# Kernel optimization log

Measured on AMD Instinct MI355X. Metric: run time of the kernel, lower is better.

Reference implementation:

```python
import jax, jax.numpy as jnp
import numpy as np

TEMPERATURE = 0.5
EPS = 1e-8  # torch CosineSimilarity eps


def setup_inputs() -> dict:
    key = jax.random.key(0)
    k1, k2 = jax.random.split(key)
    N, D = 4096, 256
    z1 = jax.random.normal(k1, (N, D), dtype=jnp.float32)
    z2 = jax.random.normal(k2, (N, D), dtype=jnp.float32)
    return {"z1": z1, "z2": z2}


def reference(z1, z2):
    N = z1.shape[0]
    z = jnp.concatenate([z1, z2], axis=0)  # [2N, D]
    # cosine similarity = normalized dot products (GEMM instead of O(N^2 D) broadcast)
    norm = jnp.linalg.norm(z, axis=-1, keepdims=True)
    zn = z / jnp.maximum(norm, EPS)
    sim = (zn @ zn.T) / TEMPERATURE  # [2N, 2N]
    # mask self-similarity on the diagonal
    idx = jnp.arange(2 * N)
    sim = jnp.where(idx[:, None] == idx[None, :], -jnp.inf, sim)
    # target[i] = (i - N) mod 2N  (arange(2N).roll(N))
    target = jnp.roll(idx, N)
    logp = jax.nn.log_softmax(sim, axis=-1)
    loss = -jnp.mean(logp[idx, target])
    return loss
```

## Files before the change

### kernel.cpp

```cpp
#include <hip/hip_runtime.h>

typedef __bf16 bf16x8 __attribute__((ext_vector_type(8)));
typedef float f32x4 __attribute__((ext_vector_type(4)));

#define TWO_LOG2E 2.88539008177792681f

#define GLOADLDS16(g, l) __builtin_amdgcn_global_load_lds(                     \
    (const __attribute__((address_space(1))) void*)(g),                        \
    (__attribute__((address_space(3))) void*)(l), 16, 0, 0)

__device__ __forceinline__ unsigned f2bf(float f) {
    unsigned u = __float_as_uint(f);
    return (u + 0x7FFFu + ((u >> 16) & 1u)) >> 16;
}

__global__ void __launch_bounds__(256) normalize_kernel(
    const float* __restrict__ z1, const float* __restrict__ z2,
    unsigned short* __restrict__ zn, float* __restrict__ S, float* __restrict__ out)
{
    if (blockIdx.x < 32) S[(blockIdx.x << 8) + threadIdx.x] = 0.f;
    if (blockIdx.x == 32 && threadIdx.x == 0) out[0] = 0.f;

    const int wave = threadIdx.x >> 6, lane = threadIdx.x & 63;
    const int row = (blockIdx.x << 2) + wave;
    const float* src = (row < 4096) ? (z1 + row * 256) : (z2 + (row - 4096) * 256);
    float4 v = ((const float4*)src)[lane];
    float ss = v.x * v.x + v.y * v.y + v.z * v.z + v.w * v.w;
#pragma unroll
    for (int m = 32; m > 0; m >>= 1) ss += __shfl_xor(ss, m, 64);
    float sc = 1.0f / fmaxf(sqrtf(ss), 1e-8f);
    uint2 w;
    w.x = f2bf(v.x * sc) | (f2bf(v.y * sc) << 16);
    w.y = f2bf(v.z * sc) | (f2bf(v.w * sc) << 16);
    *(uint2*)(zn + row * 256 + (lane << 2)) = w;
}

__global__ void __launch_bounds__(512, 4) simexp_kernel(
    const unsigned short* __restrict__ zn, float* __restrict__ S)
{
    __shared__ __align__(16) unsigned short Bs[4][2048];

    const int tid = threadIdx.x;
    const int wv = tid >> 6, lane = tid & 63;
    const int q = lane >> 4, n16 = lane & 15;
    const int g = wv >> 2, wl = wv & 3;
    const int bid = blockIdx.x;
    const int run   = ((bid & 7) << 1) | ((bid >> 3) & 1);
    const int strip = bid >> 4;
    const int rowBase = strip << 8;
    const int colRun  = run << 9;
    const int rowW = rowBase + (wv << 5);

    bf16x8 a[2][8];
#pragma unroll
    for (int rt = 0; rt < 2; ++rt)
#pragma unroll
        for (int ks = 0; ks < 8; ++ks)
            a[rt][ks] = *(const bf16x8*)(zn + ((rowW + (rt << 4) + n16) << 8)
                                            + (ks << 5) + (q << 3));

    auto stage = [&](int m) {
        const int colBase = colRun + ((m >> 2) << 5);
        const int koff = (m & 3) << 6;
        unsigned short* base = &Bs[m & 3][0];
        int s = (wl << 6) + lane;
        int c = s >> 3, d = s & 7;
        int k8 = d ^ (c & 7);
        GLOADLDS16(zn + ((colBase + c) << 8) + koff + (k8 << 3), base + (s << 3));
    };

    float rs[2][4];
#pragma unroll
    for (int i = 0; i < 2; ++i)
#pragma unroll
        for (int j = 0; j < 4; ++j) rs[i][j] = 0.f;

    f32x4 acc[2][2];
    auto consume = [&](int kc) {
        const unsigned short* bb = &Bs[kc & 3][0];
#pragma unroll
        for (int ks = 0; ks < 2; ++ks) {
            bf16x8 bf[2];
#pragma unroll
            for (int ct = 0; ct < 2; ++ct) {
                int c  = (ct << 4) + n16;
                int k8 = ((ks << 2) + q) ^ (c & 7);
                bf[ct] = *(const bf16x8*)(bb + (((c << 3) + k8) << 3));
            }
#pragma unroll
            for (int rt = 0; rt < 2; ++rt)
#pragma unroll
                for (int ct = 0; ct < 2; ++ct)
                    acc[rt][ct] = __builtin_amdgcn_mfma_f32_16x16x32_bf16(
                        a[rt][(kc << 1) + ks], bf[ct], acc[rt][ct], 0, 0, 0);
        }
    };
    auto zacc = [&]() {
#pragma unroll
        for (int rt = 0; rt < 2; ++rt)
#pragma unroll
            for (int ct = 0; ct < 2; ++ct) acc[rt][ct] = (f32x4){0.f, 0.f, 0.f, 0.f};
    };
    auto epilogue = [&]() {
#pragma unroll
        for (int rt = 0; rt < 2; ++rt)
#pragma unroll
            for (int ct = 0; ct < 2; ++ct)
#pragma unroll
                for (int r = 0; r < 4; ++r)
                    rs[rt][r] += __builtin_amdgcn_exp2f(acc[rt][ct][r] * TWO_LOG2E);
    };

    if (g == 0) stage(0); else stage(1);

    for (int cc = 0; cc < 15; ++cc) {
        zacc();
#pragma unroll
        for (int kc = 0; kc < 4; ++kc) {
            if ((kc & 1) == g) {
                stage((cc << 2) + kc + 2);
                asm volatile("s_waitcnt vmcnt(1)" ::: "memory");
            }
            __builtin_amdgcn_s_barrier();
            asm volatile("" ::: "memory");
            consume(kc);
        }
        epilogue();
    }
    zacc();
    if (g == 0) { stage(62); asm volatile("s_waitcnt vmcnt(1)" ::: "memory"); }
    __builtin_amdgcn_s_barrier();
    asm volatile("" ::: "memory");
    consume(0);
    if (g == 1) { stage(63); asm volatile("s_waitcnt vmcnt(1)" ::: "memory"); }
    __builtin_amdgcn_s_barrier();
    asm volatile("" ::: "memory");
    consume(1);
    if (g == 0) { asm volatile("s_waitcnt vmcnt(0)" ::: "memory"); }
    __builtin_amdgcn_s_barrier();
    asm volatile("" ::: "memory");
    consume(2);
    if (g == 1) { asm volatile("s_waitcnt vmcnt(0)" ::: "memory"); }
    __builtin_amdgcn_s_barrier();
    asm volatile("" ::: "memory");
    consume(3);
    epilogue();

#pragma unroll
    for (int rt = 0; rt < 2; ++rt)
#pragma unroll
        for (int r = 0; r < 4; ++r) {
            float s = rs[rt][r];
            s += __shfl_xor(s, 1, 64);
            s += __shfl_xor(s, 2, 64);
            s += __shfl_xor(s, 4, 64);
            s += __shfl_xor(s, 8, 64);
            if (n16 == 0) atomicAdd(&S[rowW + (rt << 4) + (q << 2) + r], s);
        }
}

__global__ void __launch_bounds__(256) finish_kernel(
    const unsigned short* __restrict__ zn, const float* __restrict__ S,
    float* __restrict__ out)
{
    __shared__ float vals[16];
    const int tid = threadIdx.x, lane = tid & 63, wave = tid >> 6;
    const int q = lane >> 4, n16 = lane & 15;
    const int rib = (wave << 2) + q;
    const int row = (blockIdx.x << 4) + rib;
    const int tar = (row + 4096) & 8191;

    float drr = 0.f, drt = 0.f;
#pragma unroll
    for (int i = 0; i < 4; ++i) {
        int k = (i << 6) + (n16 << 2);
        uint2 ur = *(const uint2*)(zn + (row << 8) + k);
        uint2 ut = *(const uint2*)(zn + (tar << 8) + k);
        float a0 = __uint_as_float(ur.x << 16),  a1 = __uint_as_float(ur.x & 0xFFFF0000u);
        float a2 = __uint_as_float(ur.y << 16),  a3 = __uint_as_float(ur.y & 0xFFFF0000u);
        float b0 = __uint_as_float(ut.x << 16),  b1 = __uint_as_float(ut.x & 0xFFFF0000u);
        float b2 = __uint_as_float(ut.y << 16),  b3 = __uint_as_float(ut.y & 0xFFFF0000u);
        drr += a0 * a0 + a1 * a1 + a2 * a2 + a3 * a3;
        drt += a0 * b0 + a1 * b1 + a2 * b2 + a3 * b3;
    }
#pragma unroll
    for (int m = 1; m <= 8; m <<= 1) {
        drr += __shfl_xor(drr, m, 64);
        drt += __shfl_xor(drt, m, 64);
    }
    if (n16 == 0) {
        float Sv = S[row] - __builtin_amdgcn_exp2f(drr * TWO_LOG2E);
        vals[rib] = 0.693147180559945f * __builtin_amdgcn_logf(Sv) - 2.0f * drt;
    }
    __syncthreads();
    if (tid == 0) {
        float s = 0.f;
#pragma unroll
        for (int i = 0; i < 16; ++i) s += vals[i];
        atomicAdd(out, s * (1.0f / 8192.0f));
    }
}

extern "C" void kernel_launch(void* const* d_in, const int* in_sizes, int n_in,
                              void* d_out, int out_size, void* d_ws, size_t ws_size,
                              hipStream_t stream)
{
    const float* z1 = (const float*)d_in[0];
    const float* z2 = (const float*)d_in[1];
    unsigned short* zn = (unsigned short*)d_ws;
    float* S = (float*)((char*)d_ws + 8192 * 256 * sizeof(unsigned short));
    float* out = (float*)d_out;

    normalize_kernel<<<2048, 256, 0, stream>>>(z1, z2, zn, S, out);
    simexp_kernel<<<512, 512, 0, stream>>>(zn, S);
    finish_kernel<<<512, 256, 0, stream>>>(zn, S, out);
}
```

Before: 101.6 us.

## Software-pipeline LDS fragment reads against MFMAs and raise MFMA priority

Splits the consume step into a fragment read from LDS and an MFMA step, double-buffering the B fragments so the LDS reads for chunk kc overlap the MFMAs for chunk kc-1. The epilogue exp and the accumulator reset move to the start of the next column chunk. MFMA blocks are wrapped in s_setprio to favour matrix issue. In exchange it uses more registers for the extra fragment buffer and adds explicit lgkmcnt waits before each barrier, which could reduce occupancy or serialise work.

New measurement: 135.7 us. +33.5%, slower.

```diff
diff --git a/kernel.cpp b/kernel.cpp
--- a/kernel.cpp
+++ b/kernel.cpp
@@ -76,24 +76,36 @@
         for (int j = 0; j < 4; ++j) rs[i][j] = 0.f;
 
     f32x4 acc[2][2];
-    auto consume = [&](int kc) {
+    bf16x8 bfP[2][2], bfN[2][2];
+
+    auto readfrags = [&](int kc) {
         const unsigned short* bb = &Bs[kc & 3][0];
 #pragma unroll
-        for (int ks = 0; ks < 2; ++ks) {
-            bf16x8 bf[2];
+        for (int ks = 0; ks < 2; ++ks)
 #pragma unroll
             for (int ct = 0; ct < 2; ++ct) {
                 int c  = (ct << 4) + n16;
                 int k8 = ((ks << 2) + q) ^ (c & 7);
-                bf[ct] = *(const bf16x8*)(bb + (((c << 3) + k8) << 3));
+                bfN[ks][ct] = *(const bf16x8*)(bb + (((c << 3) + k8) << 3));
             }
+    };
+    auto mfmastep = [&](int kcP) {
+        __builtin_amdgcn_s_setprio(1);
+#pragma unroll
+        for (int ks = 0; ks < 2; ++ks)
 #pragma unroll
             for (int rt = 0; rt < 2; ++rt)
 #pragma unroll
                 for (int ct = 0; ct < 2; ++ct)
                     acc[rt][ct] = __builtin_amdgcn_mfma_f32_16x16x32_bf16(
-                        a[rt][(kc << 1) + ks], bf[ct], acc[rt][ct], 0, 0, 0);
-        }
+                        a[rt][(kcP << 1) + ks], bfP[ks][ct], acc[rt][ct], 0, 0, 0);
+        __builtin_amdgcn_s_setprio(0);
+    };
+    auto rotate = [&]() {
+#pragma unroll
+        for (int ks = 0; ks < 2; ++ks)
+#pragma unroll
+            for (int ct = 0; ct < 2; ++ct) bfP[ks][ct] = bfN[ks][ct];
     };
     auto zacc = [&]() {
 #pragma unroll
@@ -111,39 +123,58 @@
                     rs[rt][r] += __builtin_amdgcn_exp2f(acc[rt][ct][r] * TWO_LOG2E);
     };
 
+    zacc();
     if (g == 0) stage(0); else stage(1);
 
     for (int cc = 0; cc < 15; ++cc) {
-        zacc();
 #pragma unroll
         for (int kc = 0; kc < 4; ++kc) {
             if ((kc & 1) == g) {
                 stage((cc << 2) + kc + 2);
                 asm volatile("s_waitcnt vmcnt(1)" ::: "memory");
             }
+            asm volatile("s_waitcnt lgkmcnt(0)" ::: "memory");
             __builtin_amdgcn_s_barrier();
             asm volatile("" ::: "memory");
-            consume(kc);
+            readfrags(kc);
+            if (kc == 0) {
+                if (cc > 0) { mfmastep(3); epilogue(); zacc(); }
+            } else {
+                mfmastep(kc - 1);
+            }
+            rotate();
         }
-        epilogue();
-    }
-    zacc();
+    }
     if (g == 0) { stage(62); asm volatile("s_waitcnt vmcnt(1)" ::: "memory"); }
-    __builtin_amdgcn_s_barrier();
-    asm volatile("" ::: "memory");
-    consume(0);
+    asm volatile("s_waitcnt lgkmcnt(0)" ::: "memory");
+    __builtin_amdgcn_s_barrier();
+    asm volatile("" ::: "memory");
+    readfrags(0);
+    mfmastep(3); epilogue(); zacc();
+    rotate();
     if (g == 1) { stage(63); asm volatile("s_waitcnt vmcnt(1)" ::: "memory"); }
-    __builtin_amdgcn_s_barrier();
-    asm volatile("" ::: "memory");
-    consume(1);
+    asm volatile("s_waitcnt lgkmcnt(0)" ::: "memory");
+    __builtin_amdgcn_s_barrier();
+    asm volatile("" ::: "memory");
+    readfrags(1);
+    mfmastep(0);
+    rotate();
     if (g == 0) { asm volatile("s_waitcnt vmcnt(0)" ::: "memory"); }
-    __builtin_amdgcn_s_barrier();
-    asm volatile("" ::: "memory");
-    consume(2);
+    asm volatile("s_waitcnt lgkmcnt(0)" ::: "memory");
+    __builtin_amdgcn_s_barrier();
+    asm volatile("" ::: "memory");
+    readfrags(2);
+    mfmastep(1);
+    rotate();
     if (g == 1) { asm volatile("s_waitcnt vmcnt(0)" ::: "memory"); }
-    __builtin_amdgcn_s_barrier();
-    asm volatile("" ::: "memory");
-    consume(3);
+    asm volatile("s_waitcnt lgkmcnt(0)" ::: "memory");
+    __builtin_amdgcn_s_barrier();
+    asm volatile("" ::: "memory");
+    readfrags(3);
+    mfmastep(2);
+    rotate();
+    asm volatile("s_waitcnt lgkmcnt(0)" ::: "memory");
+    mfmastep(3);
     epilogue();
 
 #pragma unroll
```

## Exploit symmetry of similarity matrix: compute upper-triangle tiles, accumulate row and column sums

Applied to the files above, without the earlier changes.

Switches simexp to a triangular tiling of 256x256 blocks. Off-diagonal tiles contribute exp sums to both their rows (via shuffles) and their columns (via cross-quad shuffles and atomics), and diagonal tiles skip sub-blocks below the diagonal. This roughly halves the MFMA and exp work of the dense 8192x8192 similarity. In exchange it adds column atomics and a serial loop to decode the job index, and diagonal-tile waves sit idle, which unbalances the load.

New measurement: 110.3 us. 8.5% more time.

```diff
diff --git a/kernel.cpp b/kernel.cpp
--- a/kernel.cpp
+++ b/kernel.cpp
@@ -44,119 +44,149 @@
     const int wv = tid >> 6, lane = tid & 63;
     const int q = lane >> 4, n16 = lane & 15;
     const int g = wv >> 2, wl = wv & 3;
-    const int bid = blockIdx.x;
-    const int run   = ((bid & 7) << 1) | ((bid >> 3) & 1);
-    const int strip = bid >> 4;
-    const int rowBase = strip << 8;
-    const int colRun  = run << 9;
-    const int rowW = rowBase + (wv << 5);
-
-    bf16x8 a[2][8];
-#pragma unroll
-    for (int rt = 0; rt < 2; ++rt)
-#pragma unroll
-        for (int ks = 0; ks < 8; ++ks)
-            a[rt][ks] = *(const bf16x8*)(zn + ((rowW + (rt << 4) + n16) << 8)
-                                            + (ks << 5) + (q << 3));
-
-    auto stage = [&](int m) {
-        const int colBase = colRun + ((m >> 2) << 5);
-        const int koff = (m & 3) << 6;
-        unsigned short* base = &Bs[m & 3][0];
-        int s = (wl << 6) + lane;
-        int c = s >> 3, d = s & 7;
-        int k8 = d ^ (c & 7);
-        GLOADLDS16(zn + ((colBase + c) << 8) + koff + (k8 << 3), base + (s << 3));
-    };
-
-    float rs[2][4];
-#pragma unroll
-    for (int i = 0; i < 2; ++i)
-#pragma unroll
-        for (int j = 0; j < 4; ++j) rs[i][j] = 0.f;
-
-    f32x4 acc[2][2];
-    auto consume = [&](int kc) {
-        const unsigned short* bb = &Bs[kc & 3][0];
-#pragma unroll
-        for (int ks = 0; ks < 2; ++ks) {
-            bf16x8 bf[2];
-#pragma unroll
-            for (int ct = 0; ct < 2; ++ct) {
-                int c  = (ct << 4) + n16;
-                int k8 = ((ks << 2) + q) ^ (c & 7);
-                bf[ct] = *(const bf16x8*)(bb + (((c << 3) + k8) << 3));
-            }
+
+    int ti, tj, nrep = 1;
+    {
+        int job = blockIdx.x;
+        if (job < 496) {
+            int t = 0, rem = job;
+            while (rem >= 31 - t) { rem -= 31 - t; ++t; }
+            ti = t; tj = t + 1 + rem;
+        } else {
+            ti = tj = (job - 496) << 1;
+            nrep = 2;
+        }
+    }
+
+    for (int rep = 0; rep < nrep; ++rep) {
+        const int rT = ti + rep, cT = tj + rep;
+        const bool diag = (rT == cT);
+        const int colTile = cT << 8;
+        const int rowW = (rT << 8) + (wv << 5);
+
+        bf16x8 a[2][8];
+#pragma unroll
+        for (int rt = 0; rt < 2; ++rt)
+#pragma unroll
+            for (int ks = 0; ks < 8; ++ks)
+                a[rt][ks] = *(const bf16x8*)(zn + ((rowW + (rt << 4) + n16) << 8)
+                                                + (ks << 5) + (q << 3));
+
+        auto stage = [&](int m) {
+            const int colBase = colTile + ((m >> 2) << 5);
+            const int koff = (m & 3) << 6;
+            unsigned short* base = &Bs[m & 3][0];
+            int s = (wl << 6) + lane;
+            int c = s >> 3, d = s & 7;
+            int k8 = d ^ (c & 7);
+            GLOADLDS16(zn + ((colBase + c) << 8) + koff + (k8 << 3), base + (s << 3));
+        };
+
+        float rs[2][4];
+#pragma unroll
+        for (int i = 0; i < 2; ++i)
+#pragma unroll
+            for (int j = 0; j < 4; ++j) rs[i][j] = 0.f;
+
+        f32x4 acc[2][2];
+        auto consume = [&](int kc) {
+            const unsigned short* bb = &Bs[kc & 3][0];
+#pragma unroll
+            for (int ks = 0; ks < 2; ++ks) {
+                bf16x8 bf[2];
+#pragma unroll
+                for (int ct = 0; ct < 2; ++ct) {
+                    int c  = (ct << 4) + n16;
+                    int k8 = ((ks << 2) + q) ^ (c & 7);
+                    bf[ct] = *(const bf16x8*)(bb + (((c << 3) + k8) << 3));
+                }
+#pragma unroll
+                for (int rt = 0; rt < 2; ++rt)
+#pragma unroll
+                    for (int ct = 0; ct < 2; ++ct)
+                        acc[rt][ct] = __builtin_amdgcn_mfma_f32_16x16x32_bf16(
+                            a[rt][(kc << 1) + ks], bf[ct], acc[rt][ct], 0, 0, 0);
+            }
+        };
+        auto zacc = [&]() {
 #pragma unroll
             for (int rt = 0; rt < 2; ++rt)
 #pragma unroll
+                for (int ct = 0; ct < 2; ++ct) acc[rt][ct] = (f32x4){0.f, 0.f, 0.f, 0.f};
+        };
+        auto epiRC = [&](bool doCol, int ccc) {
+            float cs[2] = {0.f, 0.f};
+#pragma unroll
+            for (int rt = 0; rt < 2; ++rt)
+#pragma unroll
                 for (int ct = 0; ct < 2; ++ct)
-                    acc[rt][ct] = __builtin_amdgcn_mfma_f32_16x16x32_bf16(
-                        a[rt][(kc << 1) + ks], bf[ct], acc[rt][ct], 0, 0, 0);
+#pragma unroll
+                    for (int r = 0; r < 4; ++r) {
+                        float e = __builtin_amdgcn_exp2f(acc[rt][ct][r] * TWO_LOG2E);
+                        rs[rt][r] += e;
+                        cs[ct] += e;
+                    }
+            if (doCol) {
+#pragma unroll
+                for (int ct = 0; ct < 2; ++ct) {
+                    float s = cs[ct];
+                    s += __shfl_xor(s, 16, 64);
+                    s += __shfl_xor(s, 32, 64);
+                    if (lane < 16)
+                        atomicAdd(&S[colTile + (ccc << 5) + (ct << 4) + n16], s);
+                }
+            }
+        };
+
+        if (g == 0) stage(0); else stage(1);
+
+        for (int cc = 0; cc < 7; ++cc) {
+            zacc();
+            const bool act   = !diag || (cc >= wv);
+            const bool doCol = !diag || (cc >  wv);
+#pragma unroll
+            for (int kc = 0; kc < 4; ++kc) {
+                if ((kc & 1) == g) {
+                    stage((cc << 2) + kc + 2);
+                    asm volatile("s_waitcnt vmcnt(1)" ::: "memory");
+                }
+                __builtin_amdgcn_s_barrier();
+                asm volatile("" ::: "memory");
+                if (act) consume(kc);
+            }
+            if (act) epiRC(doCol, cc);
         }
-    };
-    auto zacc = [&]() {
+        zacc();
+        if (g == 0) { stage(30); asm volatile("s_waitcnt vmcnt(1)" ::: "memory"); }
+        __builtin_amdgcn_s_barrier();
+        asm volatile("" ::: "memory");
+        consume(0);
+        if (g == 1) { stage(31); asm volatile("s_waitcnt vmcnt(1)" ::: "memory"); }
+        __builtin_amdgcn_s_barrier();
+        asm volatile("" ::: "memory");
+        consume(1);
+        if (g == 0) { asm volatile("s_waitcnt vmcnt(0)" ::: "memory"); }
+        __builtin_amdgcn_s_barrier();
+        asm volatile("" ::: "memory");
+        consume(2);
+        if (g == 1) { asm volatile("s_waitcnt vmcnt(0)" ::: "memory"); }
+        __builtin_amdgcn_s_barrier();
+        asm volatile("" ::: "memory");
+        consume(3);
+        epiRC(!diag || (wv < 7), 7);
+
 #pragma unroll
         for (int rt = 0; rt < 2; ++rt)
 #pragma unroll
-            for (int ct = 0; ct < 2; ++ct) acc[rt][ct] = (f32x4){0.f, 0.f, 0.f, 0.f};
-    };
-    auto epilogue = [&]() {
-#pragma unroll
-        for (int rt = 0; rt < 2; ++rt)
-#pragma unroll
-            for (int ct = 0; ct < 2; ++ct)
-#pragma unroll
-                for (int r = 0; r < 4; ++r)
-                    rs[rt][r] += __builtin_amdgcn_exp2f(acc[rt][ct][r] * TWO_LOG2E);
-    };
-
-    if (g == 0) stage(0); else stage(1);
-
-    for (int cc = 0; cc < 15; ++cc) {
-        zacc();
-#pragma unroll
-        for (int kc = 0; kc < 4; ++kc) {
-            if ((kc & 1) == g) {
-                stage((cc << 2) + kc + 2);
-                asm volatile("s_waitcnt vmcnt(1)" ::: "memory");
-            }
-            __builtin_amdgcn_s_barrier();
-            asm volatile("" ::: "memory");
-            consume(kc);
-        }
-        epilogue();
-    }
-    zacc();
-    if (g == 0) { stage(62); asm volatile("s_waitcnt vmcnt(1)" ::: "memory"); }
-    __builtin_amdgcn_s_barrier();
-    asm volatile("" ::: "memory");
-    consume(0);
-    if (g == 1) { stage(63); asm volatile("s_waitcnt vmcnt(1)" ::: "memory"); }
-    __builtin_amdgcn_s_barrier();
-    asm volatile("" ::: "memory");
-    consume(1);
-    if (g == 0) { asm volatile("s_waitcnt vmcnt(0)" ::: "memory"); }
-    __builtin_amdgcn_s_barrier();
-    asm volatile("" ::: "memory");
-    consume(2);
-    if (g == 1) { asm volatile("s_waitcnt vmcnt(0)" ::: "memory"); }
-    __builtin_amdgcn_s_barrier();
-    asm volatile("" ::: "memory");
-    consume(3);
-    epilogue();
-
-#pragma unroll
-    for (int rt = 0; rt < 2; ++rt)
-#pragma unroll
-        for (int r = 0; r < 4; ++r) {
-            float s = rs[rt][r];
-            s += __shfl_xor(s, 1, 64);
-            s += __shfl_xor(s, 2, 64);
-            s += __shfl_xor(s, 4, 64);
-            s += __shfl_xor(s, 8, 64);
-            if (n16 == 0) atomicAdd(&S[rowW + (rt << 4) + (q << 2) + r], s);
-        }
+            for (int r = 0; r < 4; ++r) {
+                float s = rs[rt][r];
+                s += __shfl_xor(s, 1, 64);
+                s += __shfl_xor(s, 2, 64);
+                s += __shfl_xor(s, 4, 64);
+                s += __shfl_xor(s, 8, 64);
+                if (n16 == 0) atomicAdd(&S[rowW + (rt << 4) + (q << 2) + r], s);
+            }
+    }
 }
 
 __global__ void __launch_bounds__(256) finish_kernel(
```
